# Kernel tuning notes

Measured on AMD Instinct MI355X. Metric: run time of the kernel, lower is better.

## Reference

```python
import jax, jax.numpy as jnp
import numpy as np
import math

B, S, DIN, E, H, WIN = 2, 2048, 512, 512, 8, 256
HD = E // H


def setup_inputs() -> dict:
    key = jax.random.key(0)
    k0, k1, k2, k3 = jax.random.split(key, 4)
    x = jax.random.normal(k0, (B, S, DIN), jnp.float32)
    padding_mask = jax.random.randint(k1, (B, S), 0, 2).astype(jnp.int32)
    # xavier-ish scale so attention logits are reasonable
    w_qkv = jax.random.normal(k2, (3 * E, DIN), jnp.float32) * (1.0 / math.sqrt(DIN))
    b_qkv = jnp.zeros((3 * E,), jnp.float32)
    w_o = jax.random.normal(k3, (E, E), jnp.float32) * (1.0 / math.sqrt(E))
    b_o = jnp.zeros((E,), jnp.float32)
    return {"x": x, "padding_mask": padding_mask, "w_qkv": w_qkv, "b_qkv": b_qkv,
            "w_o": w_o, "b_o": b_o}


def reference(x, padding_mask, w_qkv, b_qkv, w_o, b_o):
    b, s, _ = x.shape
    qkv = x @ w_qkv.T + b_qkv                     # [B,S,3E]
    qkv = qkv.reshape(b, s, H, 3 * HD).transpose(0, 2, 1, 3)  # [B,H,S,3hd]
    q, k, v = jnp.split(qkv, 3, axis=-1)          # each [B,H,S,hd]

    scale = 1.0 / math.sqrt(HD)                   # function scales by sqrt(head_dim)
    scores = jnp.einsum('bhqd,bhkd->bhqk', q, k) * scale  # [B,H,S,S]

    # Torch ref scatter_adds windowed scores into a zeros(S,S) matrix; zero-padded
    # keys contribute exactly 0 at clamped indices, so this equals band-masking.
    i = jnp.arange(s)[:, None]
    j = jnp.arange(s)[None, :]
    band = jnp.abs(i - j) <= WIN // 2             # [S,S]
    scores = jnp.where(band, scores, 0.0)
    # torch: atten_scores[atten_scores == 0.0] = -inf (kills off-band and exact zeros)
    scores = jnp.where(scores == 0.0, -jnp.inf, scores)
    # torch detaches the scores before softmax
    scores = jax.lax.stop_gradient(scores)

    key_mask = padding_mask[:, None, None, :] == 0    # [B,1,1,S]
    qry_mask = padding_mask[:, None, :, None] == 0    # [B,1,S,1]
    scores = jnp.where(key_mask, -jnp.inf, scores)
    scores = jnp.where(qry_mask, -jnp.inf, scores)

    attn = jax.nn.softmax(scores, axis=-1)
    attn = jnp.where(jnp.isnan(attn), 0.0, attn)   # fully-masked rows -> 0

    vals = jnp.einsum('bhqk,bhkd->bhqd', attn, v)  # [B,H,S,hd]
    vals = vals.transpose(0, 2, 1, 3).reshape(b, s, E)
    return vals @ w_o.T + b_o


if __name__ == '__main__':
    out = reference(**setup_inputs())
    print(out.shape)
```

## Files before the change

### kernel.cpp

```cpp
#include <hip/hip_runtime.h>
#include <math.h>

#define B 2
#define S 2048
#define H 8
#define HD 64
#define E 512
#define N3E 1536
#define M 4096
#define HALF 128

typedef unsigned short u16;
typedef unsigned int u32;
using short8 = __attribute__((ext_vector_type(8))) short;
using f32x4  = __attribute__((ext_vector_type(4))) float;

__device__ __forceinline__ u32 bfhi(float v) {
    union { float f; u32 u; } c; c.f = v;
    return (c.u + 0x7fffu + ((c.u >> 16) & 1u)) >> 16;
}
__device__ __forceinline__ float bff(u32 b) {
    union { u32 u; float f; } c; c.u = b << 16; return c.f;
}


__global__ __launch_bounds__(256) void prep_all(
    const float* __restrict__ x,    u16* __restrict__ XAh,
    const float* __restrict__ wqkv, u16* __restrict__ WBh,
    const float* __restrict__ wo,   u16* __restrict__ OBh)
{
    const int wv = threadIdx.x >> 6, ln = threadIdx.x & 63;
    const float* src; u16* dh; int Ti;
    if (blockIdx.x < 1024)      { src = x;    dh = XAh; Ti = blockIdx.x * 4 + wv; }
    else if (blockIdx.x < 1408) { src = wqkv; dh = WBh; Ti = (blockIdx.x - 1024) * 4 + wv; }
    else                        { src = wo;   dh = OBh; Ti = (blockIdx.x - 1408) * 4 + wv; }

    const int rt = Ti >> 4, kb = Ti & 15;
    const int row = rt * 16 + (ln & 15);
    const int kc  = kb * 32 + (ln >> 4) * 8;
    const float4* s = (const float4*)(src + (size_t)row * 512 + kc);
    float4 v0 = s[0], v1 = s[1];
    float f[8] = {v0.x, v0.y, v0.z, v0.w, v1.x, v1.y, v1.z, v1.w};
    short8 hs;
    #pragma unroll
    for (int e = 0; e < 8; ++e) hs[e] = (short)bfhi(f[e]);
    *(short8*)(dh + (size_t)Ti * 512 + ln * 8) = hs;
}

__global__ __launch_bounds__(256) void qkv_mfma(
    const u16* __restrict__ XAh, const u16* __restrict__ WBh,
    const float* __restrict__ bias, const int* __restrict__ mask,
    u16* __restrict__ Qh, u16* __restrict__ Kh, u16* __restrict__ Vth)
{
    const int lin = blockIdx.x;
    const int c = lin & 7, rest = lin >> 3;
    const int bx = rest & 15;
    const int by = (rest >> 4) * 8 + c;

    const int wv = threadIdx.x >> 6, ln = threadIdx.x & 63;
    const int waveM = wv >> 1, waveN = wv & 1;
    const int mtb = by * 8 + waveM * 4;
    const int ntb = bx * 6 + waveN * 3;
    const int lr = ln & 15, lk = ln >> 4;

    f32x4 acc[4][3] = {};

    for (int kb = 0; kb < 16; ++kb) {
        short8 a_h[4], b_h[3];
        #pragma unroll
        for (int i = 0; i < 4; ++i)
            a_h[i] = *(const short8*)(XAh + ((size_t)(mtb + i) * 16 + kb) * 512 + ln * 8);
        #pragma unroll
        for (int j = 0; j < 3; ++j)
            b_h[j] = *(const short8*)(WBh + ((size_t)(ntb + j) * 16 + kb) * 512 + ln * 8);
        #pragma unroll
        for (int i = 0; i < 4; ++i)
            #pragma unroll
            for (int j = 0; j < 3; ++j)
                acc[i][j] = __builtin_amdgcn_mfma_f32_16x16x32_bf16(a_h[i], b_h[j], acc[i][j], 0, 0, 0);
    }

    int rmask[4][4];
    #pragma unroll
    for (int i = 0; i < 4; ++i) {
        const int mb = (mtb + i) * 16 + lk * 4;
        #pragma unroll
        for (int r = 0; r < 4; ++r) rmask[i][r] = mask[mb + r];
    }

    #pragma unroll
    for (int j = 0; j < 3; ++j) {
        const int n  = (ntb + j) * 16 + lr;
        const int h  = n / 192;
        const int rr = n % 192;
        const int wh = rr >> 6;
        const int d  = rr & 63;
        const float bv = bias[n];
        #pragma unroll
        for (int i = 0; i < 4; ++i) {
            const int mbase = (mtb + i) * 16 + lk * 4;
            const int b_ = mbase >> 11;
            const int s0 = mbase & 2047;
            u32 hb[4];
            #pragma unroll
            for (int r = 0; r < 4; ++r) {
                float val = acc[i][j][r] + bv;
                if (wh < 2 && rmask[i][r] == 0) val = 0.f;
                hb[r] = bfhi(val);
            }
            if (wh == 0) {
                #pragma unroll
                for (int r = 0; r < 4; ++r)
                    Qh[(size_t)(mbase + r) * 512 + h * 64 + d] = (u16)hb[r];
            } else if (wh == 1) {
                #pragma unroll
                for (int r = 0; r < 4; ++r)
                    Kh[((size_t)(b_ * 8 + h) * 2048 + s0 + r) * 64 + d] = (u16)hb[r];
            } else {
                short4 h4;
                h4.x = (short)hb[0]; h4.y = (short)hb[1];
                h4.z = (short)hb[2]; h4.w = (short)hb[3];
                *(short4*)(Vth + ((size_t)(b_ * 8 + h) * 64 + d) * 2048 + s0) = h4;
            }
        }
    }
}

__global__ __launch_bounds__(512, 8) void attn_mfma(
    const u16* __restrict__ Qh, const u16* __restrict__ Kh,
    const u16* __restrict__ Vth, u16* __restrict__ VF)
{
    __shared__ u16   scb[32 * 296];
    __shared__ float rowsum[32];

    const int tid = threadIdx.x;
    const int wv = tid >> 6, ln = tid & 63;
    const int lr = ln & 15, lk = ln >> 4;
    const int bh = blockIdx.x & 15;
    const int i0 = (blockIdx.x >> 4) * 32;
    const int b = bh >> 3, h = bh & 7;

    const int klo = max(0, i0 - HALF);
    const int khi = min(S - 1, i0 + 31 + HALF);
    const int kcount = khi - klo + 1;
    const int nkt = kcount >> 4, nks = kcount >> 5;

    if (tid < 32) rowsum[tid] = 0.f;
    __syncthreads();

    const int mi = wv >> 2;

    short8 qa_h[2];
    {
        const int q = i0 + mi * 16 + lr;
        #pragma unroll
        for (int dh = 0; dh < 2; ++dh)
            qa_h[dh] = *(const short8*)(Qh + (size_t)(b * S + q) * 512 + h * 64 + dh * 32 + lk * 8);
    }

    float psum[4] = {0.f, 0.f, 0.f, 0.f};
    for (int ni = (wv & 3); ni < nkt; ni += 4) {
        const int key = klo + ni * 16 + lr;
        f32x4 acc = {};
        #pragma unroll
        for (int dh = 0; dh < 2; ++dh) {
            short8 kh_ = *(const short8*)(Kh + ((size_t)(b * 8 + h) * 2048 + key) * 64 + dh * 32 + lk * 8);
            acc = __builtin_amdgcn_mfma_f32_16x16x32_bf16(qa_h[dh], kh_, acc, 0, 0, 0);
        }
        #pragma unroll
        for (int r = 0; r < 4; ++r) {
            const int row = mi * 16 + lk * 4 + r;
            const int qr  = i0 + row;
            float s = acc[r] * 0.125f;
            const bool valid = ((u32)(key - qr + HALF) <= 2 * HALF) && (s != 0.0f);
            float p = valid ? __expf(s) : 0.f;
            u32 pb = bfhi(p);
            scb[row * 296 + ni * 16 + lr] = (u16)pb;
            psum[r] += bff(pb);
        }
    }
    #pragma unroll
    for (int off = 1; off <= 8; off <<= 1)
        #pragma unroll
        for (int r = 0; r < 4; ++r)
            psum[r] += __shfl_xor(psum[r], off);
    if (lr == 0) {
        #pragma unroll
        for (int r = 0; r < 4; ++r)
            atomicAdd(&rowsum[mi * 16 + lk * 4 + r], psum[r]);
    }
    __syncthreads();

    const int d0 = (wv & 3) * 16;
    f32x4 acc2 = {};
    for (int ks = 0; ks < nks; ++ks) {
        short8 pa = *(const short8*)&scb[(mi * 16 + lr) * 296 + ks * 32 + lk * 8];
        const size_t vo = ((size_t)(b * 8 + h) * 64 + d0 + lr) * 2048 + klo + ks * 32 + lk * 8;
        short8 vh = *(const short8*)(Vth + vo);
        acc2 = __builtin_amdgcn_mfma_f32_16x16x32_bf16(pa, vh, acc2, 0, 0, 0);
    }

    #pragma unroll
    for (int r = 0; r < 4; ++r) {
        const int row = mi * 16 + lk * 4 + r;
        const float rs = rowsum[row];
        const float inv = (rs > 0.f) ? 1.f / rs : 0.f;
        const int m = b * S + i0 + row;
        const int mt = m >> 4, lrm = m & 15;
        const int e = h * 64 + d0 + lr;
        const int kb = e >> 5, rem = e & 31;
        VF[((size_t)(mt * 16 + kb) * 64 + (rem >> 3) * 16 + lrm) * 8 + (rem & 7)]
            = (u16)bfhi(acc2[r] * inv);
    }
}

__global__ __launch_bounds__(256) void outproj_mfma(
    const u16* __restrict__ VF, const u16* __restrict__ OBh,
    const float* __restrict__ bo, float* __restrict__ out)
{
    const int lin = blockIdx.x;
    const int c = lin & 7, rest = lin >> 3;
    const int bx = rest & 7;
    const int by = (rest >> 3) * 8 + c;

    const int wv = threadIdx.x >> 6, ln = threadIdx.x & 63;
    const int waveM = wv >> 1, waveN = wv & 1;
    const int mtb = by * 8 + waveM * 4;
    const int ntb = bx * 4 + waveN * 2;
    const int lr = ln & 15, lk = ln >> 4;

    f32x4 acc[4][2] = {};

    for (int kb = 0; kb < 16; ++kb) {
        short8 a[4], b_h[2];
        #pragma unroll
        for (int i = 0; i < 4; ++i)
            a[i] = *(const short8*)(VF + ((size_t)(mtb + i) * 16 + kb) * 512 + ln * 8);
        #pragma unroll
        for (int j = 0; j < 2; ++j)
            b_h[j] = *(const short8*)(OBh + ((size_t)(ntb + j) * 16 + kb) * 512 + ln * 8);
        #pragma unroll
        for (int i = 0; i < 4; ++i)
            #pragma unroll
            for (int j = 0; j < 2; ++j)
                acc[i][j] = __builtin_amdgcn_mfma_f32_16x16x32_bf16(a[i], b_h[j], acc[i][j], 0, 0, 0);
    }

    #pragma unroll
    for (int j = 0; j < 2; ++j) {
        const int n = (ntb + j) * 16 + lr;
        const float bv = bo[n];
        #pragma unroll
        for (int i = 0; i < 4; ++i)
            #pragma unroll
            for (int r = 0; r < 4; ++r) {
                const int m = (mtb + i) * 16 + lk * 4 + r;
                out[(size_t)m * 512 + n] = acc[i][j][r] + bv;
            }
    }
}

extern "C" void kernel_launch(void* const* d_in, const int* in_sizes, int n_in,
                              void* d_out, int out_size, void* d_ws, size_t ws_size,
                              hipStream_t stream)
{
    const float* x     = (const float*)d_in[0];
    const int*   pmask = (const int*)d_in[1];
    const float* w_qkv = (const float*)d_in[2];
    const float* b_qkv = (const float*)d_in[3];
    const float* w_o   = (const float*)d_in[4];
    const float* b_o   = (const float*)d_in[5];
    float* out = (float*)d_out;

    u16* XAh = (u16*)d_out;

    char* w8 = (char*)d_ws;
    u16* WBh = (u16*)(w8 + 0);
    u16* OBh = (u16*)(w8 + 3145728);
    u16* Qh  = (u16*)(w8 + 4194304);
    u16* Kh  = (u16*)(w8 + 12582912);
    u16* Vth = (u16*)(w8 + 20971520);
    u16* VF  = (u16*)(w8 + 29360128);

    prep_all<<<1536, 256, 0, stream>>>(x, XAh, w_qkv, WBh, w_o, OBh);
    qkv_mfma<<<512, 256, 0, stream>>>(XAh, WBh, b_qkv, pmask, Qh, Kh, Vth);
    attn_mfma<<<1024, 512, 0, stream>>>(Qh, Kh, Vth, VF);
    outproj_mfma<<<256, 256, 0, stream>>>(VF, OBh, b_o, out);
}
```

Measured before the change: 119.1 us.

## Store Q, K, V in MFMA fragment-native tiled layout for contiguous attention loads

The QKV projection now writes Q, K and V directly in the per-lane fragment order the 16x16x32 bf16 MFMA consumes, tiled per (batch, head) and per 16- or 32-row tile. The attention kernel can then load each operand fragment as one contiguous 16-byte-per-lane read indexed by lane id, instead of strided row gathers. This is meant to coalesce the attention kernel's global loads. In exchange the projection epilogue's Q/K stores become scattered 2-byte writes, and the index arithmetic grows more complex.

```diff
diff --git a/kernel.cpp b/kernel.cpp
--- a/kernel.cpp
+++ b/kernel.cpp
@@ -50,7 +50,7 @@
 __global__ __launch_bounds__(256) void qkv_mfma(
     const u16* __restrict__ XAh, const u16* __restrict__ WBh,
     const float* __restrict__ bias, const int* __restrict__ mask,
-    u16* __restrict__ Qh, u16* __restrict__ Kh, u16* __restrict__ Vth)
+    u16* __restrict__ QF, u16* __restrict__ KF, u16* __restrict__ VB)
 {
     const int lin = blockIdx.x;
     const int c = lin & 7, rest = lin >> 3;
@@ -101,6 +101,7 @@
             const int mbase = (mtb + i) * 16 + lk * 4;
             const int b_ = mbase >> 11;
             const int s0 = mbase & 2047;
+            const int bh = b_ * 8 + h;
             u32 hb[4];
             #pragma unroll
             for (int r = 0; r < 4; ++r) {
@@ -108,27 +109,37 @@
                 if (wh < 2 && rmask[i][r] == 0) val = 0.f;
                 hb[r] = bfhi(val);
             }
-            if (wh == 0) {
+            if (wh < 2) {
+                const int dh_  = d >> 5;
+                const int kgrp = (d & 31) >> 3;
+                const int jj   = d & 7;
+                const int tt   = s0 >> 4;
+                const int lane0 = kgrp * 16 + lk * 4;
+                u16* dst = (wh == 0) ? QF : KF;
+                const size_t basea =
+                    (((size_t)bh * 128 + tt) * 2 + dh_) * 512 + jj;
                 #pragma unroll
                 for (int r = 0; r < 4; ++r)
-                    Qh[(size_t)(mbase + r) * 512 + h * 64 + d] = (u16)hb[r];
-            } else if (wh == 1) {
-                #pragma unroll
-                for (int r = 0; r < 4; ++r)
-                    Kh[((size_t)(b_ * 8 + h) * 2048 + s0 + r) * 64 + d] = (u16)hb[r];
+                    dst[basea + (size_t)(lane0 + r) * 8] = (u16)hb[r];
             } else {
+                const int st  = s0 >> 5;
+                const int dt  = d >> 4;
+                const int sb0 = s0 & 31;
+                const int lane_v = ((sb0 >> 3) << 4) | (d & 15);
+                const int j0  = sb0 & 7;
                 short4 h4;
                 h4.x = (short)hb[0]; h4.y = (short)hb[1];
                 h4.z = (short)hb[2]; h4.w = (short)hb[3];
-                *(short4*)(Vth + ((size_t)(b_ * 8 + h) * 64 + d) * 2048 + s0) = h4;
+                *(short4*)(VB + (((size_t)bh * 64 + st) * 4 + dt) * 512
+                              + lane_v * 8 + j0) = h4;
             }
         }
     }
 }
 
 __global__ __launch_bounds__(512, 8) void attn_mfma(
-    const u16* __restrict__ Qh, const u16* __restrict__ Kh,
-    const u16* __restrict__ Vth, u16* __restrict__ VF)
+    const u16* __restrict__ QF, const u16* __restrict__ KF,
+    const u16* __restrict__ VB, u16* __restrict__ VF)
 {
     __shared__ u16   scb[32 * 296];
     __shared__ float rowsum[32];
@@ -138,12 +149,12 @@
     const int lr = ln & 15, lk = ln >> 4;
     const int bh = blockIdx.x & 15;
     const int i0 = (blockIdx.x >> 4) * 32;
-    const int b = bh >> 3, h = bh & 7;
 
     const int klo = max(0, i0 - HALF);
     const int khi = min(S - 1, i0 + 31 + HALF);
     const int kcount = khi - klo + 1;
     const int nkt = kcount >> 4, nks = kcount >> 5;
+    const int kt0 = klo >> 4, st0 = klo >> 5;
 
     if (tid < 32) rowsum[tid] = 0.f;
     __syncthreads();
@@ -152,10 +163,10 @@
 
     short8 qa_h[2];
     {
-        const int q = i0 + mi * 16 + lr;
+        const int qt = (i0 >> 4) + mi;
         #pragma unroll
         for (int dh = 0; dh < 2; ++dh)
-            qa_h[dh] = *(const short8*)(Qh + (size_t)(b * S + q) * 512 + h * 64 + dh * 32 + lk * 8);
+            qa_h[dh] = *(const short8*)(QF + (((size_t)bh * 128 + qt) * 2 + dh) * 512 + ln * 8);
     }
 
     float psum[4] = {0.f, 0.f, 0.f, 0.f};
@@ -164,7 +175,7 @@
         f32x4 acc = {};
         #pragma unroll
         for (int dh = 0; dh < 2; ++dh) {
-            short8 kh_ = *(const short8*)(Kh + ((size_t)(b * 8 + h) * 2048 + key) * 64 + dh * 32 + lk * 8);
+            short8 kh_ = *(const short8*)(KF + (((size_t)bh * 128 + kt0 + ni) * 2 + dh) * 512 + ln * 8);
             acc = __builtin_amdgcn_mfma_f32_16x16x32_bf16(qa_h[dh], kh_, acc, 0, 0, 0);
         }
         #pragma unroll
@@ -191,15 +202,15 @@
     }
     __syncthreads();
 
-    const int d0 = (wv & 3) * 16;
+    const int dt = wv & 3;
     f32x4 acc2 = {};
     for (int ks = 0; ks < nks; ++ks) {
         short8 pa = *(const short8*)&scb[(mi * 16 + lr) * 296 + ks * 32 + lk * 8];
-        const size_t vo = ((size_t)(b * 8 + h) * 64 + d0 + lr) * 2048 + klo + ks * 32 + lk * 8;
-        short8 vh = *(const short8*)(Vth + vo);
+        short8 vh = *(const short8*)(VB + (((size_t)bh * 64 + st0 + ks) * 4 + dt) * 512 + ln * 8);
         acc2 = __builtin_amdgcn_mfma_f32_16x16x32_bf16(pa, vh, acc2, 0, 0, 0);
     }
 
+    const int b = bh >> 3, h = bh & 7;
     #pragma unroll
     for (int r = 0; r < 4; ++r) {
         const int row = mi * 16 + lk * 4 + r;
@@ -207,7 +218,7 @@
         const float inv = (rs > 0.f) ? 1.f / rs : 0.f;
         const int m = b * S + i0 + row;
         const int mt = m >> 4, lrm = m & 15;
-        const int e = h * 64 + d0 + lr;
+        const int e = h * 64 + dt * 16 + lr;
         const int kb = e >> 5, rem = e & 31;
         VF[((size_t)(mt * 16 + kb) * 64 + (rem >> 3) * 16 + lrm) * 8 + (rem & 7)]
             = (u16)bfhi(acc2[r] * inv);
@@ -277,13 +288,13 @@
     char* w8 = (char*)d_ws;
     u16* WBh = (u16*)(w8 + 0);
     u16* OBh = (u16*)(w8 + 3145728);
-    u16* Qh  = (u16*)(w8 + 4194304);
-    u16* Kh  = (u16*)(w8 + 12582912);
-    u16* Vth = (u16*)(w8 + 20971520);
+    u16* QF  = (u16*)(w8 + 4194304);
+    u16* KF  = (u16*)(w8 + 12582912);
+    u16* VB  = (u16*)(w8 + 20971520);
     u16* VF  = (u16*)(w8 + 29360128);
 
     prep_all<<<1536, 256, 0, stream>>>(x, XAh, w_qkv, WBh, w_o, OBh);
-    qkv_mfma<<<512, 256, 0, stream>>>(XAh, WBh, b_qkv, pmask, Qh, Kh, Vth);
-    attn_mfma<<<1024, 512, 0, stream>>>(Qh, Kh, Vth, VF);
+    qkv_mfma<<<512, 256, 0, stream>>>(XAh, WBh, b_qkv, pmask, QF, KF, VB);
+    attn_mfma<<<1024, 512, 0, stream>>>(QF, KF, VB, VF);
     outproj_mfma<<<256, 256, 0, stream>>>(VF, OBh, b_o, out);
 }
```

New measurement: 109.5 us. 1.09x faster.
